# Optimization experiments

Measured on AMD Instinct MI355X. Metric: run time of the kernel, lower is better.

The kernel has to match this reference:

```python
import jax, jax.numpy as jnp
import numpy as np

B, V, F = 64, 4096, 16
A, P, NF = 8, 16, 16  # n_aggregators, n_propagate, n_filters


def setup_inputs() -> dict:
    key = jax.random.key(0)
    ks = jax.random.split(key, 6)
    data = jax.random.normal(ks[0], (B, V, F), dtype=jnp.float32)
    num_vertex = jax.random.randint(ks[1], (B, 1), 1, V + 1, dtype=jnp.int32)
    W_flr = jax.random.normal(ks[2], (F, P), dtype=jnp.float32) * (1.0 / np.sqrt(F))
    b_flr = jnp.zeros((P,), jnp.float32)
    W_s = jax.random.normal(ks[3], (F, A), dtype=jnp.float32) * (1.0 / np.sqrt(F))
    b_s = jnp.zeros((A,), jnp.float32)
    W_out = jax.random.normal(ks[4], (A * P, NF), dtype=jnp.float32) * (1.0 / np.sqrt(A * P))
    b_out = jnp.zeros((NF,), jnp.float32)
    return {"data": data, "num_vertex": num_vertex, "W_flr": W_flr, "b_flr": b_flr,
            "W_s": W_s, "b_s": b_s, "W_out": W_out, "b_out": b_out}


def reference(data, num_vertex, W_flr, b_flr, W_s, b_s, W_out, b_out):
    # vertex mask: [B, V, 1], 1.0 where index < num_vertex
    idx = jnp.arange(V, dtype=jnp.int32)[None, :]          # [1, V]
    mask = (idx < num_vertex).astype(jnp.float32)[..., None]  # [B, V, 1]

    features = data @ W_flr + b_flr                         # [B, V, P]
    distance = data @ W_s + b_s                             # [B, V, A]
    edge_weights = mask * jnp.exp(-jnp.square(distance))    # [B, V, A]

    # aggregated mean over vertices: mean_v(ew[b,v,a] * feat[b,v,p]) -> [B, A, P]
    aggregated = jnp.einsum('bva,bvp->bap', edge_weights, features) / V

    # broadcast back: ew[b,v,a] * agg[b,a,p] -> [B, V, A, P] -> [B, V, A*P]
    updated = (edge_weights[:, :, :, None] * aggregated[:, None, :, :]).reshape(B, V, A * P)

    out = mask * (updated @ W_out + b_out)                  # [B, V, NF], linear activation
    return out
```

## Files before the change

### kernel.cpp

```cpp
#include <hip/hip_runtime.h>


#define B_ 64
#define V_ 4096
#define F_ 16
#define A_ 8
#define P_ 16
#define NF_ 16
#define SPLIT1 8
#define SPLIT2 16
#define GE_ (A_*F_ + A_)
#define ESTR 12
#define DSTR 20

typedef unsigned int uint32;
typedef unsigned short u16;

__device__ __forceinline__ float bflo(uint32 u){ union{uint32 i;float f;}x; x.i=u<<16; return x.f; }
__device__ __forceinline__ float bfhi(uint32 u){ union{uint32 i;float f;}x; x.i=u&0xffff0000u; return x.f; }

__device__ __forceinline__ bool detect_bf16(const void* data){
  const uint32* w = (const uint32*)data;
  int c = 0;
  #pragma unroll
  for (int i=0;i<16;++i){
    uint32 e = (w[i]>>7) & 0xffu;
    c += (e>=100u && e<=135u) ? 1 : 0;
  }
  return c >= 11;
}

template<bool BF16>
__device__ __forceinline__ float ldw(const void* p, int i){
  return BF16 ? bflo((uint32)((const u16*)p)[i]) : ((const float*)p)[i];
}

template<bool BF16>
__device__ __forceinline__ void load_vertex(const void* base, size_t v, float* d){
  if (BF16){
    const uint4* p = (const uint4*)((const u16*)base + v*F_);
    uint4 r0=p[0], r1=p[1];
    d[0]=bflo(r0.x); d[1]=bfhi(r0.x); d[2]=bflo(r0.y); d[3]=bfhi(r0.y);
    d[4]=bflo(r0.z); d[5]=bfhi(r0.z); d[6]=bflo(r0.w); d[7]=bfhi(r0.w);
    d[8]=bflo(r1.x); d[9]=bfhi(r1.x); d[10]=bflo(r1.y); d[11]=bfhi(r1.y);
    d[12]=bflo(r1.z); d[13]=bfhi(r1.z); d[14]=bflo(r1.w); d[15]=bfhi(r1.w);
  } else {
    const float4* p = (const float4*)((const float*)base + v*F_);
    float4 a=p[0], b=p[1], c=p[2], e=p[3];
    d[0]=a.x; d[1]=a.y; d[2]=a.z; d[3]=a.w;
    d[4]=b.x; d[5]=b.y; d[6]=b.z; d[7]=b.w;
    d[8]=c.x; d[9]=c.y; d[10]=c.z; d[11]=c.w;
    d[12]=e.x; d[13]=e.y; d[14]=e.z; d[15]=e.w;
  }
}

template<bool BF16>
__device__ __forceinline__ void agg_body(
    const void* __restrict__ data, const int* __restrict__ nv,
    const void* __restrict__ Ws, const void* __restrict__ bs,
    float* __restrict__ partial, uint4* __restrict__ ecache)
{
  __shared__ __align__(16) float sWs[F_*A_];
  __shared__ float sbs[A_];
  __shared__ __align__(16) float e_lds[256*ESTR];
  __shared__ __align__(16) float d_lds[256*DSTR];
  __shared__ __align__(16) float gred[8*32*4];
  __shared__ float ered2[16*8];

  const int tid = threadIdx.x;
  if (tid < F_*A_) sWs[tid] = ldw<BF16>(Ws, tid);
  if (tid < A_)    sbs[tid] = ldw<BF16>(bs, tid);
  const int b = blockIdx.x >> 3;
  const int s = blockIdx.x & 7;
  const int nvb = nv[b];
  __syncthreads();

  const int vbase = s*(V_/SPLIT1);
  const size_t voff = (size_t)b*V_ + vbase;

  const int g  = tid & 31;
  const int c  = tid >> 5;
  const int ga = g >> 2;
  const int gf = g & 3;

  float acc0=0.f, acc1=0.f, acc2=0.f, acc3=0.f;
  float E[A_];
  #pragma unroll
  for (int a=0;a<A_;++a) E[a]=0.f;

  #pragma unroll
  for (int T=0; T<2; ++T) {
    const int vl = T*256 + tid;
    float d0[16];
    load_vertex<BF16>(data, voff+vl, d0);
    const float m = (vbase+vl < nvb) ? 1.f : 0.f;

    float t0[A_];
    #pragma unroll
    for (int a=0;a<A_;++a) t0[a]=sbs[a];
    #pragma unroll
    for (int f=0; f<F_; ++f){
      const float4 w0 = *(const float4*)&sWs[f*A_];
      const float4 w1 = *(const float4*)&sWs[f*A_+4];
      const float wa[8] = {w0.x,w0.y,w0.z,w0.w,w1.x,w1.y,w1.z,w1.w};
      #pragma unroll
      for (int a=0;a<A_;++a) t0[a] = fmaf(d0[f], wa[a], t0[a]);
    }
    float e0[A_];
    #pragma unroll
    for (int a=0;a<A_;++a){
      e0[a] = m*__expf(-t0[a]*t0[a]);
      E[a] += e0[a];
    }
    {
      const uint32 q0 = __float2uint_rn(e0[0]*65535.f) | (__float2uint_rn(e0[1]*65535.f)<<16);
      const uint32 q1 = __float2uint_rn(e0[2]*65535.f) | (__float2uint_rn(e0[3]*65535.f)<<16);
      const uint32 q2 = __float2uint_rn(e0[4]*65535.f) | (__float2uint_rn(e0[5]*65535.f)<<16);
      const uint32 q3 = __float2uint_rn(e0[6]*65535.f) | (__float2uint_rn(e0[7]*65535.f)<<16);
      ecache[voff+vl] = make_uint4(q0,q1,q2,q3);
    }
    float* er = &e_lds[tid*ESTR];
    *(float4*)(er)   = make_float4(e0[0],e0[1],e0[2],e0[3]);
    *(float4*)(er+4) = make_float4(e0[4],e0[5],e0[6],e0[7]);
    float* dr = &d_lds[tid*DSTR];
    *(float4*)(dr)    = make_float4(d0[0],d0[1],d0[2],d0[3]);
    *(float4*)(dr+4)  = make_float4(d0[4],d0[5],d0[6],d0[7]);
    *(float4*)(dr+8)  = make_float4(d0[8],d0[9],d0[10],d0[11]);
    *(float4*)(dr+12) = make_float4(d0[12],d0[13],d0[14],d0[15]);
    __syncthreads();

    const float* ep = &e_lds[(c<<5)*ESTR + ga];
    const float* dp = &d_lds[(c<<5)*DSTR + gf*4];
    #pragma unroll 8
    for (int i=0;i<32;++i){
      const float e  = ep[i*ESTR];
      const float4 dv = *(const float4*)(dp + i*DSTR);
      acc0 = fmaf(e, dv.x, acc0);
      acc1 = fmaf(e, dv.y, acc1);
      acc2 = fmaf(e, dv.z, acc2);
      acc3 = fmaf(e, dv.w, acc3);
    }
    __syncthreads();
  }

  *(float4*)&gred[(c*32+g)*4] = make_float4(acc0,acc1,acc2,acc3);
  float* er = &e_lds[tid*ESTR];
  *(float4*)(er)   = make_float4(E[0],E[1],E[2],E[3]);
  *(float4*)(er+4) = make_float4(E[4],E[5],E[6],E[7]);
  __syncthreads();

  if (tid < 128){
    const int gg = tid >> 2, fi = tid & 3;
    float sum = 0.f;
    #pragma unroll
    for (int k=0;k<8;++k) sum += gred[(k*32+gg)*4 + fi];
    partial[(size_t)blockIdx.x*GE_ + (gg>>2)*F_ + (gg&3)*4 + fi] = sum;
  } else {
    const int t2 = tid - 128;
    const int q = t2 >> 3, a = t2 & 7;
    float sum = 0.f;
    #pragma unroll
    for (int i=0;i<16;++i) sum += e_lds[(q*16+i)*ESTR + a];
    ered2[q*8 + a] = sum;
  }
  __syncthreads();
  if (tid < A_){
    float sum = 0.f;
    #pragma unroll
    for (int q=0;q<16;++q) sum += ered2[q*8 + tid];
    partial[(size_t)blockIdx.x*GE_ + A_*F_ + tid] = sum;
  }
}

__global__ __launch_bounds__(256, 4) void k_agg(
    const void* __restrict__ data, const int* __restrict__ nv,
    const void* __restrict__ Ws, const void* __restrict__ bs,
    float* __restrict__ partial, uint4* __restrict__ ecache)
{
  if (detect_bf16(data)) agg_body<true >(data, nv, Ws, bs, partial, ecache);
  else                   agg_body<false>(data, nv, Ws, bs, partial, ecache);
}

template<bool BF16>
__device__ __forceinline__ void out_body(
    const int* __restrict__ nv,
    const void* __restrict__ Wflr, const void* __restrict__ bflr,
    const void* __restrict__ Wout, const void* __restrict__ bout,
    const float* __restrict__ partial, const uint4* __restrict__ ecache,
    float* __restrict__ out)
{
  __shared__ __align__(16) float sWf[F_*P_];
  __shared__ __align__(16) float sWo[A_*P_*NF_];
  __shared__ float sbf[P_], sbo[NF_];
  __shared__ float sGE[GE_];
  __shared__ float sagg[A_*P_];
  __shared__ __align__(16) float sM[A_*NF_];

  const int tid = threadIdx.x;
  const int b = blockIdx.x >> 4;
  const int s = blockIdx.x & 15;

  sWf[tid] = ldw<BF16>(Wflr, tid);
  #pragma unroll
  for (int j=0;j<8;++j)
    sWo[tid*8+j] = ldw<BF16>(Wout, tid*8+j);
  if (tid < P_)  sbf[tid] = ldw<BF16>(bflr, tid);
  if (tid < NF_) sbo[tid] = ldw<BF16>(bout, tid);
  if (tid < GE_) {
    const float* pp = partial + (size_t)(b*SPLIT1)*GE_ + tid;
    float v = 0.f;
    #pragma unroll
    for (int k=0;k<SPLIT1;++k) v += pp[(size_t)k*GE_];
    sGE[tid] = v;
  }
  const int nvb = nv[b];
  __syncthreads();

  if (tid < A_*P_) {
    const int a = tid >> 4, p = tid & 15;
    float acc = sGE[A_*F_ + a] * sbf[p];
    #pragma unroll
    for (int f=0;f<F_;++f) acc = fmaf(sGE[a*F_+f], sWf[f*P_+p], acc);
    sagg[tid] = acc * (1.0f/(float)V_);
  }
  __syncthreads();
  if (tid < A_*NF_) {
    const int a = tid >> 4, n = tid & 15;
    float m = 0.f;
    #pragma unroll
    for (int p=0;p<P_;++p)
      m = fmaf(sagg[a*P_+p], sWo[(a*P_+p)*NF_+n], m);
    sM[tid] = m;
  }
  __syncthreads();

  const int vbase = s*(V_/SPLIT2);
  const int vl = tid;
  const size_t v = (size_t)b*V_ + vbase + vl;
  const float m = (vbase+vl < nvb) ? 1.f : 0.f;

  const uint4 eu = ecache[v];
  const float k16 = 1.0f/65535.f;
  float e0[A_];
  e0[0] = (float)(eu.x & 0xffffu)*k16;  e0[1] = (float)(eu.x >> 16)*k16;
  e0[2] = (float)(eu.y & 0xffffu)*k16;  e0[3] = (float)(eu.y >> 16)*k16;
  e0[4] = (float)(eu.z & 0xffffu)*k16;  e0[5] = (float)(eu.z >> 16)*k16;
  e0[6] = (float)(eu.w & 0xffffu)*k16;  e0[7] = (float)(eu.w >> 16)*k16;

  float o[NF_];
  #pragma unroll
  for (int n=0;n<NF_;++n) o[n] = m*sbo[n];
  #pragma unroll
  for (int a=0;a<A_;++a){
    const float e = e0[a];
    const float4 q0 = *(const float4*)&sM[a*NF_];
    const float4 q1 = *(const float4*)&sM[a*NF_+4];
    const float4 q2 = *(const float4*)&sM[a*NF_+8];
    const float4 q3 = *(const float4*)&sM[a*NF_+12];
    const float ma[16] = {q0.x,q0.y,q0.z,q0.w, q1.x,q1.y,q1.z,q1.w,
                          q2.x,q2.y,q2.z,q2.w, q3.x,q3.y,q3.z,q3.w};
    #pragma unroll
    for (int n=0;n<NF_;++n) o[n] = fmaf(e, ma[n], o[n]);
  }

  float4* ob = (float4*)(out + v*NF_);
  ob[0] = make_float4(o[0],  o[1],  o[2],  o[3]);
  ob[1] = make_float4(o[4],  o[5],  o[6],  o[7]);
  ob[2] = make_float4(o[8],  o[9],  o[10], o[11]);
  ob[3] = make_float4(o[12], o[13], o[14], o[15]);
}

__global__ __launch_bounds__(256, 4) void k_out(
    const void* __restrict__ data, const int* __restrict__ nv,
    const void* __restrict__ Wflr, const void* __restrict__ bflr,
    const void* __restrict__ Wout, const void* __restrict__ bout,
    const float* __restrict__ partial, const uint4* __restrict__ ecache,
    float* __restrict__ out)
{
  if (detect_bf16(data))
    out_body<true >(nv, Wflr, bflr, Wout, bout, partial, ecache, out);
  else
    out_body<false>(nv, Wflr, bflr, Wout, bout, partial, ecache, out);
}

extern "C" void kernel_launch(void* const* d_in, const int* in_sizes, int n_in,
                              void* d_out, int out_size, void* d_ws, size_t ws_size,
                              hipStream_t stream) {
  const void* data = d_in[0];
  const int*  nv   = (const int*)d_in[1];
  const void* Wflr = d_in[2];
  const void* bflr = d_in[3];
  const void* Ws   = d_in[4];
  const void* bs   = d_in[5];
  const void* Wout = d_in[6];
  const void* bout = d_in[7];
  float* out = (float*)d_out;
  float* partial = (float*)d_ws;
  uint4* ecache  = (uint4*)((char*)d_ws + 278528);

  hipLaunchKernelGGL(k_agg, dim3(B_*SPLIT1), dim3(256), 0, stream,
                     data, nv, Ws, bs, partial, ecache);
  hipLaunchKernelGGL(k_out, dim3(B_*SPLIT2), dim3(256), 0, stream,
                     data, nv, Wflr, bflr, Wout, bout, partial, ecache, out);
}
```

Measured before the change: 94.06 us.

## Register-tile aggregation reduction, coalesce output stores, drop weight LDS staging

```diff
diff --git a/kernel.cpp b/kernel.cpp
--- a/kernel.cpp
+++ b/kernel.cpp
@@ -8,10 +8,11 @@
 #define P_ 16
 #define NF_ 16
 #define SPLIT1 8
-#define SPLIT2 16
+#define SPLIT2 8
 #define GE_ (A_*F_ + A_)
 #define ESTR 12
 #define DSTR 20
+#define GSL 132
 
 typedef unsigned int uint32;
 typedef unsigned short u16;
@@ -60,30 +61,28 @@
     const void* __restrict__ Ws, const void* __restrict__ bs,
     float* __restrict__ partial, uint4* __restrict__ ecache)
 {
-  __shared__ __align__(16) float sWs[F_*A_];
-  __shared__ float sbs[A_];
   __shared__ __align__(16) float e_lds[256*ESTR];
   __shared__ __align__(16) float d_lds[256*DSTR];
-  __shared__ __align__(16) float gred[8*32*4];
+  __shared__ __align__(16) float gred[32*GSL];
   __shared__ float ered2[16*8];
 
   const int tid = threadIdx.x;
-  if (tid < F_*A_) sWs[tid] = ldw<BF16>(Ws, tid);
-  if (tid < A_)    sbs[tid] = ldw<BF16>(bs, tid);
   const int b = blockIdx.x >> 3;
   const int s = blockIdx.x & 7;
   const int nvb = nv[b];
-  __syncthreads();
 
   const int vbase = s*(V_/SPLIT1);
   const size_t voff = (size_t)b*V_ + vbase;
 
-  const int g  = tid & 31;
-  const int c  = tid >> 5;
-  const int ga = g >> 2;
-  const int gf = g & 3;
-
-  float acc0=0.f, acc1=0.f, acc2=0.f, acc3=0.f;
+  const int g   = tid & 7;
+  const int c   = tid >> 3;
+  const int ga2 = g >> 2;
+  const int gf  = g & 3;
+
+  float4 acc0 = make_float4(0,0,0,0);
+  float4 acc1 = make_float4(0,0,0,0);
+  float4 acc2 = make_float4(0,0,0,0);
+  float4 acc3 = make_float4(0,0,0,0);
   float E[A_];
   #pragma unroll
   for (int a=0;a<A_;++a) E[a]=0.f;
@@ -97,14 +96,13 @@
 
     float t0[A_];
     #pragma unroll
-    for (int a=0;a<A_;++a) t0[a]=sbs[a];
+    for (int a=0;a<A_;++a) t0[a] = ldw<BF16>(bs, a);
     #pragma unroll
     for (int f=0; f<F_; ++f){
-      const float4 w0 = *(const float4*)&sWs[f*A_];
-      const float4 w1 = *(const float4*)&sWs[f*A_+4];
-      const float wa[8] = {w0.x,w0.y,w0.z,w0.w,w1.x,w1.y,w1.z,w1.w};
+      const float df = d0[f];
       #pragma unroll
-      for (int a=0;a<A_;++a) t0[a] = fmaf(d0[f], wa[a], t0[a]);
+      for (int a=0;a<A_;++a)
+        t0[a] = fmaf(df, ldw<BF16>(Ws, f*A_+a), t0[a]);
     }
     float e0[A_];
     #pragma unroll
@@ -129,32 +127,43 @@
     *(float4*)(dr+12) = make_float4(d0[12],d0[13],d0[14],d0[15]);
     __syncthreads();
 
-    const float* ep = &e_lds[(c<<5)*ESTR + ga];
-    const float* dp = &d_lds[(c<<5)*DSTR + gf*4];
-    #pragma unroll 8
-    for (int i=0;i<32;++i){
-      const float e  = ep[i*ESTR];
-      const float4 dv = *(const float4*)(dp + i*DSTR);
-      acc0 = fmaf(e, dv.x, acc0);
-      acc1 = fmaf(e, dv.y, acc1);
-      acc2 = fmaf(e, dv.z, acc2);
-      acc3 = fmaf(e, dv.w, acc3);
+    #pragma unroll
+    for (int i=0;i<8;++i){
+      const int v = c + (i<<5);
+      const float4 e4 = *(const float4*)&e_lds[v*ESTR + ga2*4];
+      const float4 d4 = *(const float4*)&d_lds[v*DSTR + gf*4];
+      acc0.x = fmaf(e4.x, d4.x, acc0.x); acc0.y = fmaf(e4.x, d4.y, acc0.y);
+      acc0.z = fmaf(e4.x, d4.z, acc0.z); acc0.w = fmaf(e4.x, d4.w, acc0.w);
+      acc1.x = fmaf(e4.y, d4.x, acc1.x); acc1.y = fmaf(e4.y, d4.y, acc1.y);
+      acc1.z = fmaf(e4.y, d4.z, acc1.z); acc1.w = fmaf(e4.y, d4.w, acc1.w);
+      acc2.x = fmaf(e4.z, d4.x, acc2.x); acc2.y = fmaf(e4.z, d4.y, acc2.y);
+      acc2.z = fmaf(e4.z, d4.z, acc2.z); acc2.w = fmaf(e4.z, d4.w, acc2.w);
+      acc3.x = fmaf(e4.w, d4.x, acc3.x); acc3.y = fmaf(e4.w, d4.y, acc3.y);
+      acc3.z = fmaf(e4.w, d4.z, acc3.z); acc3.w = fmaf(e4.w, d4.w, acc3.w);
     }
     __syncthreads();
   }
 
-  *(float4*)&gred[(c*32+g)*4] = make_float4(acc0,acc1,acc2,acc3);
+  {
+    float* gb = &gred[c*GSL + g*16];
+    *(float4*)(gb)    = acc0;
+    *(float4*)(gb+4)  = acc1;
+    *(float4*)(gb+8)  = acc2;
+    *(float4*)(gb+12) = acc3;
+  }
   float* er = &e_lds[tid*ESTR];
   *(float4*)(er)   = make_float4(E[0],E[1],E[2],E[3]);
   *(float4*)(er+4) = make_float4(E[4],E[5],E[6],E[7]);
   __syncthreads();
 
   if (tid < 128){
-    const int gg = tid >> 2, fi = tid & 3;
+    const int a = tid >> 4, f = tid & 15;
+    const int gg = (a>>2)*4 + (f>>2);
+    const int idx = (a&3)*4 + (f&3);
     float sum = 0.f;
-    #pragma unroll
-    for (int k=0;k<8;++k) sum += gred[(k*32+gg)*4 + fi];
-    partial[(size_t)blockIdx.x*GE_ + (gg>>2)*F_ + (gg&3)*4 + fi] = sum;
+    #pragma unroll 8
+    for (int cc=0;cc<32;++cc) sum += gred[cc*GSL + gg*16 + idx];
+    partial[(size_t)blockIdx.x*GE_ + a*F_ + f] = sum;
   } else {
     const int t2 = tid - 128;
     const int q = t2 >> 3, a = t2 & 7;
@@ -172,7 +181,7 @@
   }
 }
 
-__global__ __launch_bounds__(256, 4) void k_agg(
+__global__ __launch_bounds__(256, 2) void k_agg(
     const void* __restrict__ data, const int* __restrict__ nv,
     const void* __restrict__ Ws, const void* __restrict__ bs,
     float* __restrict__ partial, uint4* __restrict__ ecache)
@@ -189,23 +198,14 @@
     const float* __restrict__ partial, const uint4* __restrict__ ecache,
     float* __restrict__ out)
 {
-  __shared__ __align__(16) float sWf[F_*P_];
-  __shared__ __align__(16) float sWo[A_*P_*NF_];
-  __shared__ float sbf[P_], sbo[NF_];
   __shared__ float sGE[GE_];
   __shared__ float sagg[A_*P_];
   __shared__ __align__(16) float sM[A_*NF_];
 
   const int tid = threadIdx.x;
-  const int b = blockIdx.x >> 4;
-  const int s = blockIdx.x & 15;
-
-  sWf[tid] = ldw<BF16>(Wflr, tid);
-  #pragma unroll
-  for (int j=0;j<8;++j)
-    sWo[tid*8+j] = ldw<BF16>(Wout, tid*8+j);
-  if (tid < P_)  sbf[tid] = ldw<BF16>(bflr, tid);
-  if (tid < NF_) sbo[tid] = ldw<BF16>(bout, tid);
+  const int b = blockIdx.x >> 3;
+  const int s = blockIdx.x & 7;
+
   if (tid < GE_) {
     const float* pp = partial + (size_t)(b*SPLIT1)*GE_ + tid;
     float v = 0.f;
@@ -218,9 +218,9 @@
 
   if (tid < A_*P_) {
     const int a = tid >> 4, p = tid & 15;
-    float acc = sGE[A_*F_ + a] * sbf[p];
-    #pragma unroll
-    for (int f=0;f<F_;++f) acc = fmaf(sGE[a*F_+f], sWf[f*P_+p], acc);
+    float acc = sGE[A_*F_ + a] * ldw<BF16>(bflr, p);
+    #pragma unroll
+    for (int f=0;f<F_;++f) acc = fmaf(sGE[a*F_+f], ldw<BF16>(Wflr, f*P_+p), acc);
     sagg[tid] = acc * (1.0f/(float)V_);
   }
   __syncthreads();
@@ -229,48 +229,47 @@
     float m = 0.f;
     #pragma unroll
     for (int p=0;p<P_;++p)
-      m = fmaf(sagg[a*P_+p], sWo[(a*P_+p)*NF_+n], m);
+      m = fmaf(sagg[a*P_+p], ldw<BF16>(Wout, (a*P_+p)*NF_+n), m);
     sM[tid] = m;
   }
   __syncthreads();
 
+  const int vg = tid >> 2, nq = tid & 3;
+  float4 Mq[A_];
+  #pragma unroll
+  for (int a=0;a<A_;++a) Mq[a] = *(const float4*)&sM[a*NF_ + nq*4];
+  const float4 bo4 = make_float4(ldw<BF16>(bout,nq*4), ldw<BF16>(bout,nq*4+1),
+                                 ldw<BF16>(bout,nq*4+2), ldw<BF16>(bout,nq*4+3));
+
   const int vbase = s*(V_/SPLIT2);
-  const int vl = tid;
-  const size_t v = (size_t)b*V_ + vbase + vl;
-  const float m = (vbase+vl < nvb) ? 1.f : 0.f;
-
-  const uint4 eu = ecache[v];
+  const size_t voff = (size_t)b*V_ + vbase;
   const float k16 = 1.0f/65535.f;
-  float e0[A_];
-  e0[0] = (float)(eu.x & 0xffffu)*k16;  e0[1] = (float)(eu.x >> 16)*k16;
-  e0[2] = (float)(eu.y & 0xffffu)*k16;  e0[3] = (float)(eu.y >> 16)*k16;
-  e0[4] = (float)(eu.z & 0xffffu)*k16;  e0[5] = (float)(eu.z >> 16)*k16;
-  e0[6] = (float)(eu.w & 0xffffu)*k16;  e0[7] = (float)(eu.w >> 16)*k16;
-
-  float o[NF_];
-  #pragma unroll
-  for (int n=0;n<NF_;++n) o[n] = m*sbo[n];
-  #pragma unroll
-  for (int a=0;a<A_;++a){
-    const float e = e0[a];
-    const float4 q0 = *(const float4*)&sM[a*NF_];
-    const float4 q1 = *(const float4*)&sM[a*NF_+4];
-    const float4 q2 = *(const float4*)&sM[a*NF_+8];
-    const float4 q3 = *(const float4*)&sM[a*NF_+12];
-    const float ma[16] = {q0.x,q0.y,q0.z,q0.w, q1.x,q1.y,q1.z,q1.w,
-                          q2.x,q2.y,q2.z,q2.w, q3.x,q3.y,q3.z,q3.w};
-    #pragma unroll
-    for (int n=0;n<NF_;++n) o[n] = fmaf(e, ma[n], o[n]);
-  }
-
-  float4* ob = (float4*)(out + v*NF_);
-  ob[0] = make_float4(o[0],  o[1],  o[2],  o[3]);
-  ob[1] = make_float4(o[4],  o[5],  o[6],  o[7]);
-  ob[2] = make_float4(o[8],  o[9],  o[10], o[11]);
-  ob[3] = make_float4(o[12], o[13], o[14], o[15]);
-}
-
-__global__ __launch_bounds__(256, 4) void k_out(
+
+  #pragma unroll
+  for (int i=0;i<8;++i){
+    const int vl = vg + (i<<6);
+    const size_t v = voff + vl;
+    const float m = (vbase+vl < nvb) ? 1.f : 0.f;
+    const uint4 eu = ecache[v];
+    float e0[A_];
+    e0[0] = (float)(eu.x & 0xffffu)*k16;  e0[1] = (float)(eu.x >> 16)*k16;
+    e0[2] = (float)(eu.y & 0xffffu)*k16;  e0[3] = (float)(eu.y >> 16)*k16;
+    e0[4] = (float)(eu.z & 0xffffu)*k16;  e0[5] = (float)(eu.z >> 16)*k16;
+    e0[6] = (float)(eu.w & 0xffffu)*k16;  e0[7] = (float)(eu.w >> 16)*k16;
+
+    float4 o = make_float4(m*bo4.x, m*bo4.y, m*bo4.z, m*bo4.w);
+    #pragma unroll
+    for (int a=0;a<A_;++a){
+      o.x = fmaf(e0[a], Mq[a].x, o.x);
+      o.y = fmaf(e0[a], Mq[a].y, o.y);
+      o.z = fmaf(e0[a], Mq[a].z, o.z);
+      o.w = fmaf(e0[a], Mq[a].w, o.w);
+    }
+    *(float4*)(out + v*NF_ + nq*4) = o;
+  }
+}
+
+__global__ __launch_bounds__(256, 2) void k_out(
     const void* __restrict__ data, const int* __restrict__ nv,
     const void* __restrict__ Wflr, const void* __restrict__ bflr,
     const void* __restrict__ Wout, const void* __restrict__ bout,
```

New measurement: 94.90 us. Within noise of the previous version (+0.9%).
